# Kernel optimization log

Hardware: AMD Instinct MI355X
Metric: run time of the kernel (lower is better)

The kernel has to match this reference:

```python
import jax, jax.numpy as jnp
import numpy as np

T, B, DIN, H, AA, L = 1024, 32, 256, 256, 21, 2


def setup_inputs() -> dict:
    key = jax.random.key(0)
    ks = jax.random.split(key, 8)
    scale = 0.05

    def rn(i, shape):
        return jax.random.normal(ks[i], shape, dtype=jnp.float32) * scale

    return {
        "x": jax.random.normal(ks[0], (B, T, DIN), dtype=jnp.float32),
        "hidden": jnp.zeros((2 * L, B, H), jnp.float32),  # accepted but unused, as in torch forward
        # layer 0: input DIN -> per-direction 4 chunks of H; layer 1: input 2H
        "w_l0": rn(1, (DIN, 2, 4, H)),
        "wc_l0": rn(2, (2, 2, H)),            # [dir, (v_f, v_r), H]
        "b_l0": jnp.zeros((2, 2, H), jnp.float32),  # [dir, (b_f, b_r), H]
        "w_l1": rn(3, (2 * H, 2, 4, H)),
        "wc_l1": rn(4, (2, 2, H)),
        "b_l1": jnp.zeros((2, 2, H), jnp.float32),
        "fc1_w": rn(5, (H, 2 * H)),
        "fc1_b": jnp.zeros((H,), jnp.float32),
        "lp_w": rn(6, (AA, H)),
        "lp_b": jnp.zeros((AA,), jnp.float32),
    }


def _sru_scan(u, vf, vr, bf, br):
    # u: (T, B, 4, H) with chunks [candidate, forget, reset, highway]
    def step(c, ut):
        f = jax.nn.sigmoid(ut[:, 1] + vf * c + bf)
        c2 = f * c + (1.0 - f) * ut[:, 0]
        r = jax.nn.sigmoid(ut[:, 2] + vr * c + br)
        h = r * c2 + (1.0 - r) * ut[:, 3]
        return c2, h

    c0 = jnp.zeros((u.shape[1], u.shape[-1]), u.dtype)
    _, hs = jax.lax.scan(step, c0, u)
    return hs  # (T, B, H)


def _sru_layer(x, w, wc, b):
    # x: (T, B, Din); w: (Din, 2, 4, H)
    U = jnp.einsum('tbd,dnkh->tbnkh', x, w)
    hf = _sru_scan(U[:, :, 0], wc[0, 0], wc[0, 1], b[0, 0], b[0, 1])
    hb = _sru_scan(U[::-1, :, 1], wc[1, 0], wc[1, 1], b[1, 0], b[1, 1])[::-1]
    return jnp.concatenate([hf, hb], axis=-1)  # (T, B, 2H)


def reference(x, hidden, w_l0, wc_l0, b_l0, w_l1, wc_l1, b_l1, fc1_w, fc1_b, lp_w, lp_b):
    h = jnp.transpose(x, (1, 0, 2))  # (T, B, DIN)
    h = _sru_layer(h, w_l0, wc_l0, b_l0)
    h = _sru_layer(h, w_l1, wc_l1, b_l1)
    h = jnp.transpose(h, (1, 0, 2))  # (B, T, 2H)
    h = h @ fc1_w.T + fc1_b
    logits = h @ lp_w.T + lp_b
    return jax.nn.log_softmax(logits, axis=-1)  # (B, T, AA)
```

## Files before the change

kernel.cpp:

```cpp
#include <hip/hip_runtime.h>
#include <hip/hip_bf16.h>

#define T_DIM 1024
#define B_DIM 32
#define DIN_DIM 256
#define H_DIM 256
#define AA_DIM 21
#define M_ROWS (B_DIM * T_DIM)

typedef __attribute__((ext_vector_type(8))) short bf16x8;
typedef __attribute__((ext_vector_type(4))) float f32x4;

typedef __attribute__((address_space(3))) void lds_void;
typedef const __attribute__((address_space(1))) void glb_void;

#define LOG2E_F 1.44269504088896340736f

__device__ __forceinline__ void gload_lds16(const void* g, void* l) {
    __builtin_amdgcn_global_load_lds((glb_void*)g, (lds_void*)l, 16, 0, 0);
}

__device__ __forceinline__ float b2f(unsigned short v) {
    unsigned u = ((unsigned)v) << 16;
    float f;
    __builtin_memcpy(&f, &u, 4);
    return f;
}

__device__ __forceinline__ unsigned short f2bu(float f) {
    __hip_bfloat16 h = __float2bfloat16(f);
    unsigned short u;
    __builtin_memcpy(&u, &h, 2);
    return u;
}

#define CVT_V0 2097152
#define CVT_N1 524288
#define CVT_N2 1048576
#define CVT_V3 32768
#define CVT_N4 8192
#define CVT_TOT (CVT_V0 + CVT_N1 + CVT_N2 + CVT_V3 + CVT_N4)
__global__ __launch_bounds__(256) void cvt_all(
    const float* __restrict__ x,  const float* __restrict__ w0,
    const float* __restrict__ w1, const float* __restrict__ fcw,
    const float* __restrict__ lpw,
    __hip_bfloat16* __restrict__ xb,  __hip_bfloat16* __restrict__ w0t,
    __hip_bfloat16* __restrict__ w1t, __hip_bfloat16* __restrict__ fcwb,
    __hip_bfloat16* __restrict__ lpwb)
{
    int i = blockIdx.x * 256 + threadIdx.x;
    if (i < CVT_V0) {
        float4 v = ((const float4*)x)[i];
        ushort4 o = { f2bu(v.x), f2bu(v.y), f2bu(v.z), f2bu(v.w) };
        ((ushort4*)xb)[i] = o;
        return;
    }
    i -= CVT_V0;
    if (i < CVT_N1) {
        int kk = i >> 11, rem = i & 2047;
        int dir = rem >> 10, k = (rem >> 8) & 3, h = rem & 255;
        w0t[(long)(dir * 1024 + h * 4 + k) * 256 + kk] = __float2bfloat16(w0[i]);
        return;
    }
    i -= CVT_N1;
    if (i < CVT_N2) {
        int kk = i >> 11, rem = i & 2047;
        int dir = rem >> 10, k = (rem >> 8) & 3, h = rem & 255;
        w1t[(long)(dir * 1024 + h * 4 + k) * 512 + kk] = __float2bfloat16(w1[i]);
        return;
    }
    i -= CVT_N2;
    if (i < CVT_V3) {
        float4 v = ((const float4*)fcw)[i];
        ushort4 o = { f2bu(v.x), f2bu(v.y), f2bu(v.z), f2bu(v.w) };
        ((ushort4*)fcwb)[i] = o;
        return;
    }
    i -= CVT_V3;
    if (i < CVT_N4) {
        int n = i >> 8, k = i & 255;
        lpwb[i] = __float2bfloat16(n < AA_DIM ? lpw[n * 256 + k] : 0.0f);
    }
}

template<int U2OUT>
__global__ __launch_bounds__(256) void gemm_bf16(
    const __hip_bfloat16* __restrict__ A,
    const __hip_bfloat16* __restrict__ Bt,
    const float* __restrict__ bias,
    __hip_bfloat16* __restrict__ C,
    int M, int N, int K, int nbShift)
{
    __shared__ __align__(16) char smb[32768];

    const int tid  = threadIdx.x;
    const int lane = tid & 63;
    const int wave = tid >> 6;
    const int wm = wave & 1;
    const int wn = wave >> 1;

    const int L   = blockIdx.x;
    const int s   = L >> 3;
    const int nb  = s & ((1 << nbShift) - 1);
    const int mb  = ((s >> nbShift) << 3) + (L & 7);
    const long n0 = (long)nb * 128;
    const long m0 = (long)mb * 128;

    f32x4 acc[4][4] = {};

    const int ldrow = lane >> 2;
    const int ldq   = lane & 3;
    const int gq    = ldq ^ ((ldrow >> 1) & 3);
    const int gkoff = gq * 8;

    const int fr = lane & 15;
    const int kq = lane >> 4;
    const int sw = (kq ^ ((fr >> 1) & 3)) * 16;

    for (int kb = 0; kb < K; kb += 64) {
        __syncthreads();
#pragma unroll
        for (int i = 0; i < 4; ++i) {
            const int cid = wave * 4 + i;
            const int rc  = cid >> 1;
            const int kh  = cid & 1;
            const long row = rc * 16 + ldrow;
            const int koff = kb + kh * 32 + gkoff;
            gload_lds16(A  + (m0 + row) * (long)K + koff,
                        smb + rc * 2048 + kh * 1024);
            gload_lds16(Bt + (n0 + row) * (long)K + koff,
                        smb + 16384 + rc * 2048 + kh * 1024);
        }
        __syncthreads();

#pragma unroll
        for (int ss = 0; ss < 2; ++ss) {
            bf16x8 af[4], bfv[4];
#pragma unroll
            for (int i = 0; i < 4; ++i) {
                af[i]  = *(const bf16x8*)(smb + (wm * 4 + i) * 2048 + ss * 1024 + fr * 64 + sw);
                bfv[i] = *(const bf16x8*)(smb + 16384 + (wn * 4 + i) * 2048 + ss * 1024 + fr * 64 + sw);
            }
#pragma unroll
            for (int i = 0; i < 4; ++i)
#pragma unroll
                for (int j = 0; j < 4; ++j)
                    acc[i][j] = __builtin_amdgcn_mfma_f32_16x16x32_bf16(
                        af[i], bfv[j], acc[i][j], 0, 0, 0);
        }
    }

    const int col_l = lane & 15;
    const int row_l = (lane >> 4) * 4;
    __hip_bfloat16* smC = (__hip_bfloat16*)smb;
#pragma unroll
    for (int p = 0; p < 2; ++p) {
        __syncthreads();
        if (wm == p) {
#pragma unroll
            for (int j = 0; j < 4; ++j) {
                const long gc = n0 + wn * 64 + j * 16 + col_l;
                const float bv = bias ? bias[gc] : 0.0f;
#pragma unroll
                for (int i = 0; i < 4; ++i)
#pragma unroll
                    for (int r = 0; r < 4; ++r)
                        smC[(i * 16 + row_l + r) * 132 + wn * 64 + j * 16 + col_l] =
                            __float2bfloat16(acc[i][j][r] + bv);
            }
        }
        __syncthreads();
        const int cb = (tid & 7) * 16;
#pragma unroll
        for (int s2 = 0; s2 < 2; ++s2) {
            const int rr = s2 * 32 + (tid >> 3);
            const long gr = m0 + p * 64 + rr;
            bf16x8 v0 = *(const bf16x8*)(smC + rr * 132 + cb);
            bf16x8 v1 = *(const bf16x8*)(smC + rr * 132 + cb + 8);
            if (U2OUT) {
                const int bI  = (int)(gr >> 10);
                const int t   = (int)(gr & 1023);
                const long gc0 = n0 + cb;
                const int dir = (int)(gc0 >> 10);
                const int hg  = ((int)gc0 >> 8) & 3;
                const int beta = bI * 8 + dir * 4 + hg;
                const long base = ((long)beta * 1024 + t) * 256 + (gc0 & 255);
                *(bf16x8*)(C + base)     = v0;
                *(bf16x8*)(C + base + 8) = v1;
            } else {
                *(bf16x8*)(C + gr * (long)N + n0 + cb)     = v0;
                *(bf16x8*)(C + gr * (long)N + n0 + cb + 8) = v1;
            }
        }
    }
}

#define SCAN_S 64
#define SCAN_NB (T_DIM / SCAN_S)
#define GRP 16

__device__ __forceinline__ float scan_step(
    uint2 u, float c, float nvf, float nvr, float nbf, float nbr,
    __hip_bfloat16* hq)
{
    float u0, u1, u2, u3;
    unsigned a0 = u.x << 16, a1 = u.x & 0xffff0000u;
    unsigned a2 = u.y << 16, a3 = u.y & 0xffff0000u;
    __builtin_memcpy(&u0, &a0, 4); __builtin_memcpy(&u1, &a1, 4);
    __builtin_memcpy(&u2, &a2, 4); __builtin_memcpy(&u3, &a3, 4);
    const float nf0 = __builtin_fmaf(-LOG2E_F, u1, nbf);
    const float nr0 = __builtin_fmaf(-LOG2E_F, u2, nbr);
    const float ef = __builtin_amdgcn_exp2f(__builtin_fmaf(nvf, c, nf0));
    const float er = __builtin_amdgcn_exp2f(__builtin_fmaf(nvr, c, nr0));
    const float f  = __builtin_amdgcn_rcpf(1.0f + ef);
    const float r  = __builtin_amdgcn_rcpf(1.0f + er);
    const float c2 = __builtin_fmaf(f, c - u0, u0);
    const float hv = __builtin_fmaf(r, c2 - u3, u3);
    *hq = __float2bfloat16(hv);
    return c2;
}

__global__ __launch_bounds__(256) void sru_scan(
    const __hip_bfloat16* __restrict__ U2,
    const float* __restrict__ wc,
    const float* __restrict__ bias,
    __hip_bfloat16* __restrict__ hout)
{
    __shared__ __align__(16) char lds[2 * SCAN_S * 512];
    const int tid  = threadIdx.x;
    const int wave = tid >> 6;
    const int lane = tid & 63;
    const int beta = blockIdx.x;
    const int b    = beta >> 3;
    const int dir  = (beta >> 2) & 1;
    const int hg   = beta & 3;
    const int h    = hg * 64 + lane;

    const char* gslice = (const char*)U2 + (size_t)beta * (1024 * 512);

    const float nvf = -LOG2E_F * wc[(dir * 2 + 0) * H_DIM + h];
    const float nvr = -LOG2E_F * wc[(dir * 2 + 1) * H_DIM + h];
    const float nbf = -LOG2E_F * bias[(dir * 2 + 0) * H_DIM + h];
    const float nbr = -LOG2E_F * bias[(dir * 2 + 1) * H_DIM + h];
    __hip_bfloat16* hp = hout + ((long)(b * 1024 + (dir ? 1023 : 0))) * 512 + dir * 256 + h;
    const long hstep = dir ? -512L : 512L;
    float c = 0.0f;

    const int plane = lane & 31;

    if (wave > 0) {
        for (int p = wave - 1; p < SCAN_S / 2; p += 3) {
            const int sl = 2 * p + (lane >> 5);
            const int t  = dir ? (1023 - sl) : sl;
            gload_lds16(gslice + (size_t)t * 512 + plane * 16, lds + p * 1024);
        }
    }
    __syncthreads();

    for (int bat = 0; bat < SCAN_NB; ++bat) {
        if (wave > 0) {
            if (bat + 1 < SCAN_NB) {
                char* halfN = lds + ((bat + 1) & 1) * (SCAN_S * 512);
                const int tb = (bat + 1) * SCAN_S;
                for (int p = wave - 1; p < SCAN_S / 2; p += 3) {
                    const int sl = tb + 2 * p + (lane >> 5);
                    const int t  = dir ? (1023 - sl) : sl;
                    gload_lds16(gslice + (size_t)t * 512 + plane * 16,
                                halfN + p * 1024);
                }
            }
        } else {
            const char* half = lds + (bat & 1) * (SCAN_S * 512);
            __hip_bfloat16* hq = hp + (long)(bat * SCAN_S) * hstep;
            uint2 qa[GRP], qb[GRP];
#pragma unroll
            for (int j = 0; j < GRP; ++j)
                qa[j] = *(const uint2*)(half + (0 * GRP + j) * 512 + (lane << 3));
#pragma unroll
            for (int j = 0; j < GRP; ++j)
                qb[j] = *(const uint2*)(half + (1 * GRP + j) * 512 + (lane << 3));
#pragma unroll
            for (int j = 0; j < GRP; ++j)
                c = scan_step(qa[j], c, nvf, nvr, nbf, nbr, hq + (long)j * hstep);
#pragma unroll
            for (int j = 0; j < GRP; ++j)
                qa[j] = *(const uint2*)(half + (2 * GRP + j) * 512 + (lane << 3));
#pragma unroll
            for (int j = 0; j < GRP; ++j)
                c = scan_step(qb[j], c, nvf, nvr, nbf, nbr, hq + (long)(GRP + j) * hstep);
#pragma unroll
            for (int j = 0; j < GRP; ++j)
                qb[j] = *(const uint2*)(half + (3 * GRP + j) * 512 + (lane << 3));
#pragma unroll
            for (int j = 0; j < GRP; ++j)
                c = scan_step(qa[j], c, nvf, nvr, nbf, nbr, hq + (long)(2 * GRP + j) * hstep);
#pragma unroll
            for (int j = 0; j < GRP; ++j)
                c = scan_step(qb[j], c, nvf, nvr, nbf, nbr, hq + (long)(3 * GRP + j) * hstep);
        }
        __syncthreads();
    }
}

__global__ __launch_bounds__(256) void logits_mfma(
    const __hip_bfloat16* __restrict__ fc,
    const __hip_bfloat16* __restrict__ lpwb,
    const float* __restrict__ lpb,
    float* __restrict__ out)
{
    __shared__ __align__(16) char smb[25088];
    const int tid  = threadIdx.x;
    const int lane = tid & 63;
    const int wave = tid >> 6;
    const long m0  = (long)blockIdx.x * 128;

    for (int idx = tid; idx < 32 * 32; idx += 256) {
        const int rw = idx >> 5, sl = idx & 31;
        *(bf16x8*)(smb + rw * 528 + sl * 16) =
            *(const bf16x8*)(lpwb + rw * 256 + sl * 8);
    }

    const int ldrow = lane >> 2;
    const int ldq   = lane & 3;
    const int gq    = ldq ^ ((ldrow >> 1) & 3);
    const int gkoff = gq * 8;

    const int fr = lane & 15;
    const int kq = lane >> 4;
    const int sw = (kq ^ ((fr >> 1) & 3)) * 16;

    f32x4 acc[2][2] = {};
    for (int kc = 0; kc < 8; ++kc) {
        __syncthreads();
#pragma unroll
        for (int i = 0; i < 2; ++i) {
            const int rc = wave * 2 + i;
            gload_lds16(fc + (m0 + rc * 16 + ldrow) * 256 + kc * 32 + gkoff,
                        smb + 16896 + rc * 1024);
        }
        __syncthreads();
        bf16x8 af[2], bfv[2];
#pragma unroll
        for (int i = 0; i < 2; ++i)
            af[i] = *(const bf16x8*)(smb + 16896 + (wave * 2 + i) * 1024 + fr * 64 + sw);
#pragma unroll
        for (int j = 0; j < 2; ++j)
            bfv[j] = *(const bf16x8*)(smb + (j * 16 + fr) * 528 + kc * 64 + kq * 16);
#pragma unroll
        for (int i = 0; i < 2; ++i)
#pragma unroll
            for (int j = 0; j < 2; ++j)
                acc[i][j] = __builtin_amdgcn_mfma_f32_16x16x32_bf16(
                    af[i], bfv[j], acc[i][j], 0, 0, 0);
    }

    __syncthreads();
    float* smC = (float*)smb;
    const int col_l = lane & 15;
    const int row_l = (lane >> 4) * 4;
#pragma unroll
    for (int j = 0; j < 2; ++j) {
        const int gc = j * 16 + col_l;
        const float bv = (gc < AA_DIM) ? lpb[gc] : 0.0f;
#pragma unroll
        for (int i = 0; i < 2; ++i)
#pragma unroll
            for (int r = 0; r < 4; ++r)
                smC[(wave * 32 + i * 16 + row_l + r) * 36 + gc] = acc[i][j][r] + bv;
    }
    __syncthreads();
    if (tid < 128) {
        const float* rowp = smC + tid * 36;
        float m = rowp[0];
#pragma unroll
        for (int a = 1; a < AA_DIM; ++a) m = fmaxf(m, rowp[a]);
        float s = 0.0f;
#pragma unroll
        for (int a = 0; a < AA_DIM; ++a) s += __expf(rowp[a] - m);
        const float lse = __logf(s) + m;
        float* op = out + (m0 + tid) * AA_DIM;
#pragma unroll
        for (int a = 0; a < AA_DIM; ++a) op[a] = rowp[a] - lse;
    }
}

extern "C" void kernel_launch(void* const* d_in, const int* in_sizes, int n_in,
                              void* d_out, int out_size, void* d_ws, size_t ws_size,
                              hipStream_t stream)
{
    const float* x     = (const float*)d_in[0];
    const float* w_l0  = (const float*)d_in[2];
    const float* wc_l0 = (const float*)d_in[3];
    const float* b_l0  = (const float*)d_in[4];
    const float* w_l1  = (const float*)d_in[5];
    const float* wc_l1 = (const float*)d_in[6];
    const float* b_l1  = (const float*)d_in[7];
    const float* fc1_w = (const float*)d_in[8];
    const float* fc1_b = (const float*)d_in[9];
    const float* lp_w  = (const float*)d_in[10];
    const float* lp_b  = (const float*)d_in[11];
    float* out = (float*)d_out;

    char* ws = (char*)d_ws;
    __hip_bfloat16* U      = (__hip_bfloat16*)(ws);
    __hip_bfloat16* h0b    = (__hip_bfloat16*)(ws + 134217728);
    __hip_bfloat16* h1b    = (__hip_bfloat16*)(ws + 167772160);
    __hip_bfloat16* xb     = (__hip_bfloat16*)(ws + 201326592);
    __hip_bfloat16* fcob   = xb;
    __hip_bfloat16* w0t    = (__hip_bfloat16*)(ws + 218103808);
    __hip_bfloat16* w1t    = (__hip_bfloat16*)(ws + 219152384);
    __hip_bfloat16* fc1wb  = (__hip_bfloat16*)(ws + 221249536);
    __hip_bfloat16* lpwb   = (__hip_bfloat16*)(ws + 221511680);

    cvt_all<<<(CVT_TOT + 255) / 256, 256, 0, stream>>>(
        x, w_l0, w_l1, fc1_w, lp_w, xb, w0t, w1t, fc1wb, lpwb);

    gemm_bf16<1><<<4096, 256, 0, stream>>>(
        xb, w0t, nullptr, U, M_ROWS, 2048, DIN_DIM, 4);
    sru_scan<<<256, 256, 0, stream>>>(U, wc_l0, b_l0, h0b);
    gemm_bf16<1><<<4096, 256, 0, stream>>>(
        h0b, w1t, nullptr, U, M_ROWS, 2048, 512, 4);
    sru_scan<<<256, 256, 0, stream>>>(U, wc_l1, b_l1, h1b);
    gemm_bf16<0><<<512, 256, 0, stream>>>(
        h1b, fc1wb, fc1_b, fcob, M_ROWS, 256, 512, 1);
    logits_mfma<<<M_ROWS / 128, 256, 0, stream>>>(fcob, lpwb, lp_b, out);
}
```

Before: 383.2 us.

## Split SRU scan gates across lane pairs using DPP exchange

The serial scan previously ran in one wave, with each lane computing both the forget and reset gates for one hidden unit. Now two waves run the recurrence, and each hidden unit is handled by a pair of lanes: one computes the forget gate, the other the reset gate, and the new cell value is exchanged through a DPP lane swap. The weight conversion reorders the gate chunks so that each lane reads one packed bf16 pair from LDS. Only two waves are left to prefetch U from global memory instead of three. This shortens the per-step dependent chain, at the cost of a cross-lane DPP operation on the critical path and fewer loader waves.

```diff
diff --git a/kernel.cpp b/kernel.cpp
--- a/kernel.cpp
+++ b/kernel.cpp
@@ -59,14 +59,16 @@
     if (i < CVT_N1) {
         int kk = i >> 11, rem = i & 2047;
         int dir = rem >> 10, k = (rem >> 8) & 3, h = rem & 255;
-        w0t[(long)(dir * 1024 + h * 4 + k) * 256 + kk] = __float2bfloat16(w0[i]);
+        int q = (k == 0) ? 1 : ((k == 1) ? 0 : k);
+        w0t[(long)(dir * 1024 + h * 4 + q) * 256 + kk] = __float2bfloat16(w0[i]);
         return;
     }
     i -= CVT_N1;
     if (i < CVT_N2) {
         int kk = i >> 11, rem = i & 2047;
         int dir = rem >> 10, k = (rem >> 8) & 3, h = rem & 255;
-        w1t[(long)(dir * 1024 + h * 4 + k) * 512 + kk] = __float2bfloat16(w1[i]);
+        int q = (k == 0) ? 1 : ((k == 1) ? 0 : k);
+        w1t[(long)(dir * 1024 + h * 4 + q) * 512 + kk] = __float2bfloat16(w1[i]);
         return;
     }
     i -= CVT_N2;
@@ -199,25 +201,29 @@
 #define SCAN_NB (T_DIM / SCAN_S)
 #define GRP 16
 
-__device__ __forceinline__ float scan_step(
-    uint2 u, float c, float nvf, float nvr, float nbf, float nbr,
+__device__ __forceinline__ float scan_step2(
+    unsigned u, float c, float nv, float nb, int role,
     __hip_bfloat16* hq)
 {
-    float u0, u1, u2, u3;
-    unsigned a0 = u.x << 16, a1 = u.x & 0xffff0000u;
-    unsigned a2 = u.y << 16, a3 = u.y & 0xffff0000u;
-    __builtin_memcpy(&u0, &a0, 4); __builtin_memcpy(&u1, &a1, 4);
-    __builtin_memcpy(&u2, &a2, 4); __builtin_memcpy(&u3, &a3, 4);
-    const float nf0 = __builtin_fmaf(-LOG2E_F, u1, nbf);
-    const float nr0 = __builtin_fmaf(-LOG2E_F, u2, nbr);
-    const float ef = __builtin_amdgcn_exp2f(__builtin_fmaf(nvf, c, nf0));
-    const float er = __builtin_amdgcn_exp2f(__builtin_fmaf(nvr, c, nr0));
-    const float f  = __builtin_amdgcn_rcpf(1.0f + ef);
-    const float r  = __builtin_amdgcn_rcpf(1.0f + er);
-    const float c2 = __builtin_fmaf(f, c - u0, u0);
-    const float hv = __builtin_fmaf(r, c2 - u3, u3);
-    *hq = __float2bfloat16(hv);
-    return c2;
+    float av, bv;
+    {
+        unsigned a = u << 16, b = u & 0xffff0000u;
+        __builtin_memcpy(&av, &a, 4);
+        __builtin_memcpy(&bv, &b, 4);
+    }
+    const float na = __builtin_fmaf(-LOG2E_F, av, nb);
+    const float e  = __builtin_amdgcn_exp2f(__builtin_fmaf(nv, c, na));
+    const float s  = __builtin_amdgcn_rcpf(1.0f + e);
+    const float cf = __builtin_fmaf(s, c - bv, bv);
+    int cfi, cni;
+    __builtin_memcpy(&cfi, &cf, 4);
+    cni = __builtin_amdgcn_update_dpp(cfi, cfi, 160 ,
+                                      0xf, 0xf, false);
+    float cn;
+    __builtin_memcpy(&cn, &cni, 4);
+    const float hv = __builtin_fmaf(s, cn - bv, bv);
+    if (role) *hq = __float2bfloat16(hv);
+    return cn;
 }
 
 __global__ __launch_bounds__(256) void sru_scan(
@@ -234,22 +240,25 @@
     const int b    = beta >> 3;
     const int dir  = (beta >> 2) & 1;
     const int hg   = beta & 3;
-    const int h    = hg * 64 + lane;
 
     const char* gslice = (const char*)U2 + (size_t)beta * (1024 * 512);
 
-    const float nvf = -LOG2E_F * wc[(dir * 2 + 0) * H_DIM + h];
-    const float nvr = -LOG2E_F * wc[(dir * 2 + 1) * H_DIM + h];
-    const float nbf = -LOG2E_F * bias[(dir * 2 + 0) * H_DIM + h];
-    const float nbr = -LOG2E_F * bias[(dir * 2 + 1) * H_DIM + h];
-    __hip_bfloat16* hp = hout + ((long)(b * 1024 + (dir ? 1023 : 0))) * 512 + dir * 256 + h;
+    const int role = lane & 1;
+    const int cl   = lane >> 1;
+    const int ci   = (wave & 1) * 32 + cl;
+    const int h    = hg * 64 + ci;
+    const float nv = -LOG2E_F * wc[(dir * 2 + role) * H_DIM + h];
+    const float nb = -LOG2E_F * bias[(dir * 2 + role) * H_DIM + h];
+    const int ldsoff = ci * 8 + role * 4;
+    __hip_bfloat16* hbase =
+        hout + ((long)(b * 1024 + (dir ? 1023 : 0))) * 512 + dir * 256 + h;
     const long hstep = dir ? -512L : 512L;
     float c = 0.0f;
 
     const int plane = lane & 31;
 
-    if (wave > 0) {
-        for (int p = wave - 1; p < SCAN_S / 2; p += 3) {
+    if (wave >= 2) {
+        for (int p = wave - 2; p < SCAN_S / 2; p += 2) {
             const int sl = 2 * p + (lane >> 5);
             const int t  = dir ? (1023 - sl) : sl;
             gload_lds16(gslice + (size_t)t * 512 + plane * 16, lds + p * 1024);
@@ -258,11 +267,11 @@
     __syncthreads();
 
     for (int bat = 0; bat < SCAN_NB; ++bat) {
-        if (wave > 0) {
+        if (wave >= 2) {
             if (bat + 1 < SCAN_NB) {
                 char* halfN = lds + ((bat + 1) & 1) * (SCAN_S * 512);
                 const int tb = (bat + 1) * SCAN_S;
-                for (int p = wave - 1; p < SCAN_S / 2; p += 3) {
+                for (int p = wave - 2; p < SCAN_S / 2; p += 2) {
                     const int sl = tb + 2 * p + (lane >> 5);
                     const int t  = dir ? (1023 - sl) : sl;
                     gload_lds16(gslice + (size_t)t * 512 + plane * 16,
@@ -271,32 +280,32 @@
             }
         } else {
             const char* half = lds + (bat & 1) * (SCAN_S * 512);
-            __hip_bfloat16* hq = hp + (long)(bat * SCAN_S) * hstep;
-            uint2 qa[GRP], qb[GRP];
-#pragma unroll
-            for (int j = 0; j < GRP; ++j)
-                qa[j] = *(const uint2*)(half + (0 * GRP + j) * 512 + (lane << 3));
-#pragma unroll
-            for (int j = 0; j < GRP; ++j)
-                qb[j] = *(const uint2*)(half + (1 * GRP + j) * 512 + (lane << 3));
-#pragma unroll
-            for (int j = 0; j < GRP; ++j)
-                c = scan_step(qa[j], c, nvf, nvr, nbf, nbr, hq + (long)j * hstep);
-#pragma unroll
-            for (int j = 0; j < GRP; ++j)
-                qa[j] = *(const uint2*)(half + (2 * GRP + j) * 512 + (lane << 3));
-#pragma unroll
-            for (int j = 0; j < GRP; ++j)
-                c = scan_step(qb[j], c, nvf, nvr, nbf, nbr, hq + (long)(GRP + j) * hstep);
-#pragma unroll
-            for (int j = 0; j < GRP; ++j)
-                qb[j] = *(const uint2*)(half + (3 * GRP + j) * 512 + (lane << 3));
-#pragma unroll
-            for (int j = 0; j < GRP; ++j)
-                c = scan_step(qa[j], c, nvf, nvr, nbf, nbr, hq + (long)(2 * GRP + j) * hstep);
-#pragma unroll
-            for (int j = 0; j < GRP; ++j)
-                c = scan_step(qb[j], c, nvf, nvr, nbf, nbr, hq + (long)(3 * GRP + j) * hstep);
+            __hip_bfloat16* hq = hbase + (long)(bat * SCAN_S) * hstep;
+            unsigned qa[GRP], qb[GRP];
+#pragma unroll
+            for (int j = 0; j < GRP; ++j)
+                qa[j] = *(const unsigned*)(half + (0 * GRP + j) * 512 + ldsoff);
+#pragma unroll
+            for (int j = 0; j < GRP; ++j)
+                qb[j] = *(const unsigned*)(half + (1 * GRP + j) * 512 + ldsoff);
+#pragma unroll
+            for (int j = 0; j < GRP; ++j)
+                c = scan_step2(qa[j], c, nv, nb, role, hq + (long)j * hstep);
+#pragma unroll
+            for (int j = 0; j < GRP; ++j)
+                qa[j] = *(const unsigned*)(half + (2 * GRP + j) * 512 + ldsoff);
+#pragma unroll
+            for (int j = 0; j < GRP; ++j)
+                c = scan_step2(qb[j], c, nv, nb, role, hq + (long)(GRP + j) * hstep);
+#pragma unroll
+            for (int j = 0; j < GRP; ++j)
+                qb[j] = *(const unsigned*)(half + (3 * GRP + j) * 512 + ldsoff);
+#pragma unroll
+            for (int j = 0; j < GRP; ++j)
+                c = scan_step2(qa[j], c, nv, nb, role, hq + (long)(2 * GRP + j) * hstep);
+#pragma unroll
+            for (int j = 0; j < GRP; ++j)
+                c = scan_step2(qb[j], c, nv, nb, role, hq + (long)(3 * GRP + j) * hstep);
         }
         __syncthreads();
     }
```

Result: slower. 410.3 us (+7.1%).
